# Performance work log

Measured on AMD Instinct MI355X. Metric: run time of the kernel, lower is better.

## Reference

```python
import jax, jax.numpy as jnp
import numpy as np

N_NODES = 100000
N_EDGES = 1600000
F_IN, F_HID, F_OUT = 48, 16, 16
K = 2  # kernel_size, dim=1, degree=1 open B-spline -> basis (1-u, u)


def glorot(key, shape):
    fan_in, fan_out = shape[-2], shape[-1]
    s = jnp.sqrt(6.0 / (fan_in + fan_out))
    return jax.random.uniform(key, shape, jnp.float32, -s, s)


def setup_inputs() -> dict:
    key = jax.random.key(0)
    ks = jax.random.split(key, 10)
    x = jax.random.normal(ks[0], (N_NODES, F_IN), jnp.float32)
    edge_attr = jax.random.uniform(ks[1], (N_EDGES, 1), jnp.float32)
    edge_index = jax.random.randint(ks[2], (2, N_EDGES), 0, N_NODES, jnp.int64)
    W1 = glorot(ks[3], (K, F_IN, F_HID))
    root1 = glorot(ks[4], (F_IN, F_HID))
    b1 = jnp.zeros((F_HID,), jnp.float32)
    W2 = glorot(ks[5], (K, F_HID, F_OUT))
    root2 = glorot(ks[6], (F_HID, F_OUT))
    b2 = jnp.zeros((F_OUT,), jnp.float32)
    return {"x": x, "edge_attr": edge_attr, "edge_index": edge_index,
            "W1": W1, "root1": root1, "b1": b1, "W2": W2, "root2": root2, "b2": b2}


def spline_conv(x, edge_index, u, W, root, bias, num_nodes):
    # x: [N,Fin], u: [E] pseudo coords in [0,1], W: [2,Fin,Fout]
    src, dst = edge_index[0], edge_index[1]
    xj = x[src]                                        # [E,Fin] gather
    m = jnp.einsum('ef,kfo->eko', xj, W)               # [E,2,Fout]
    basis = jnp.stack([1.0 - u, u], axis=1)            # linear open B-spline, K=2
    msg = jnp.einsum('ek,eko->eo', basis, m)           # [E,Fout]
    agg = jax.ops.segment_sum(msg, dst, num_segments=num_nodes)
    cnt = jax.ops.segment_sum(jnp.ones_like(msg[:, 0]), dst, num_segments=num_nodes)
    agg = agg / jnp.maximum(cnt, 1.0)[:, None]         # aggr='mean'
    return agg + x @ root + bias                       # root_weight + bias


def reference(x, edge_attr, edge_index, W1, root1, b1, W2, root2, b2):
    u = edge_attr[:, 0]
    h = jax.nn.elu(spline_conv(x, edge_index, u, W1, root1, b1, N_NODES))
    out = spline_conv(h, edge_index, u, W2, root2, b2, N_NODES)
    return jax.nn.log_softmax(out, axis=1)
```

## Files before the change

### kernel.cpp

```cpp
#include <hip/hip_runtime.h>
#include <math.h>

#define N_NODES 100000
#define N_EDGES 1600000
#define NBUK 782
#define BNODES 128
#define CAPSH 12
#define CAP 4096
#define NCHUNK 512
#define CPE 3125
#define NTBLK 1563
#define WS 52
#define RPW (BNODES + 1)

#define NTL(p) __builtin_nontemporal_load(p)

__device__ __forceinline__ unsigned bf16_rne(float x) {
    unsigned u = __float_as_uint(x);
    return (u + 0x7FFFu + ((u >> 16) & 1u)) >> 16;
}

__device__ __forceinline__ void acc4(float* acc, uint4 w, float uu) {
    acc[0] += fmaf(uu, __uint_as_float(w.x & 0xFFFF0000u), __uint_as_float(w.x << 16));
    acc[1] += fmaf(uu, __uint_as_float(w.y & 0xFFFF0000u), __uint_as_float(w.y << 16));
    acc[2] += fmaf(uu, __uint_as_float(w.z & 0xFFFF0000u), __uint_as_float(w.z << 16));
    acc[3] += fmaf(uu, __uint_as_float(w.w & 0xFFFF0000u), __uint_as_float(w.w << 16));
}

__device__ __forceinline__ void edge_accum(unsigned pk,
                                           const uint4* __restrict__ YPH,
                                           float acc[16]) {
    float uu = (float)(pk >> 17) * (1.0f / 32767.0f);
    const uint4* yp = YPH + (size_t)(pk & 0x1FFFFu) * 4;
    uint4 w0 = yp[0], w1 = yp[1], w2 = yp[2], w3 = yp[3];
    acc4(acc + 0, w0, uu);
    acc4(acc + 4, w1, uu);
    acc4(acc + 8, w2, uu);
    acc4(acc + 12, w3, uu);
}

__device__ __forceinline__ void edge_accum2(unsigned p0, unsigned p1,
                                            const uint4* __restrict__ YPH,
                                            float acc[16]) {
    float u0 = (float)(p0 >> 17) * (1.0f / 32767.0f);
    float u1 = (float)(p1 >> 17) * (1.0f / 32767.0f);
    const uint4* a = YPH + (size_t)(p0 & 0x1FFFFu) * 4;
    const uint4* b = YPH + (size_t)(p1 & 0x1FFFFu) * 4;
    uint4 w0 = a[0], w1 = a[1], w2 = a[2], w3 = a[3];
    uint4 v0 = b[0], v1 = b[1], v2 = b[2], v3 = b[3];
    acc4(acc + 0, w0, u0);
    acc4(acc + 4, w1, u0);
    acc4(acc + 8, w2, u0);
    acc4(acc + 12, w3, u0);
    acc4(acc + 0, v0, u1);
    acc4(acc + 4, v1, u1);
    acc4(acc + 8, v2, u1);
    acc4(acc + 12, v3, u1);
}

__global__ __launch_bounds__(1024)
void transform1(const float* __restrict__ X,
                const float* __restrict__ W,
                const float* __restrict__ root,
                const float* __restrict__ bias,
                unsigned* __restrict__ YPH, float* __restrict__ R,
                int* __restrict__ cursor) {
    int t = threadIdx.x;
    if (blockIdx.x == NTBLK) {
        if (t < NBUK) cursor[t] = t * CAP;
        return;
    }
    __shared__ float sW0[16 * WS];
    __shared__ float sWd[16 * WS];
    __shared__ float sR[16 * WS];
    __shared__ float sB[16];
    for (int i = t; i < 48 * 16; i += 1024) {
        int f = i >> 4, o = i & 15;
        float w0 = W[i];
        float w1 = W[48 * 16 + i];
        sW0[o * WS + f] = w0;
        sWd[o * WS + f] = w1 - w0;
        sR[o * WS + f]  = root[i];
    }
    if (t < 16) sB[t] = bias[t];
    __syncthreads();

    int idx = blockIdx.x * 1024 + t;
    int n = idx >> 4;
    int o = idx & 15;
    if (n >= N_NODES) return;

    const float4* xr  = (const float4*)(X + (long)n * 48);
    const float4* w0p = (const float4*)(sW0 + o * WS);
    const float4* wdp = (const float4*)(sWd + o * WS);
    const float4* wrp = (const float4*)(sR  + o * WS);
    float a0 = 0.0f, a1 = 0.0f, ar = 0.0f;
#pragma unroll
    for (int fc = 0; fc < 12; ++fc) {
        float4 xv = xr[fc];
        float4 w0 = w0p[fc];
        float4 wd = wdp[fc];
        float4 wr = wrp[fc];
        a0 = fmaf(xv.x, w0.x, a0); a0 = fmaf(xv.y, w0.y, a0);
        a0 = fmaf(xv.z, w0.z, a0); a0 = fmaf(xv.w, w0.w, a0);
        a1 = fmaf(xv.x, wd.x, a1); a1 = fmaf(xv.y, wd.y, a1);
        a1 = fmaf(xv.z, wd.z, a1); a1 = fmaf(xv.w, wd.w, a1);
        ar = fmaf(xv.x, wr.x, ar); ar = fmaf(xv.y, wr.y, ar);
        ar = fmaf(xv.z, wr.z, ar); ar = fmaf(xv.w, wr.w, ar);
    }
    YPH[idx] = bf16_rne(a0) | (bf16_rne(a1) << 16);
    R[idx]   = ar + sB[o];
}

__global__ __launch_bounds__(1024)
void scatter_edges(const int* __restrict__ src, const int* __restrict__ dst,
                   const float* __restrict__ u,
                   int* __restrict__ cursor,
                   unsigned* __restrict__ pkb, unsigned char* __restrict__ dlb) {
    __shared__ unsigned upk[CPE];
    __shared__ unsigned short ubuk[CPE];
    __shared__ unsigned char udl[CPE];
    __shared__ unsigned spk[CPE];
    __shared__ unsigned char sdl[CPE];
    __shared__ unsigned short sbuk[CPE];
    __shared__ int lcur[NBUK];
    __shared__ int gbase[NBUK];
    __shared__ int sc[1024];

    int t = threadIdx.x, c = blockIdx.x;

    for (int i = t; i < NBUK; i += 1024) lcur[i] = 0;
    __syncthreads();
    for (int j = t; j < CPE; j += 1024) {
        int e = c * CPE + j;
        int d = NTL(dst + e);
        float uu = NTL(u + e);
        uu = uu < 0.0f ? 0.0f : (uu > 1.0f ? 1.0f : uu);
        int u15 = (int)fmaf(uu, 32767.0f, 0.5f);
        upk[j] = (unsigned)NTL(src + e) | ((unsigned)u15 << 17);
        udl[j] = (unsigned char)(d & 127);
        int b = d >> 7;
        ubuk[j] = (unsigned short)b;
        atomicAdd(&lcur[b], 1);
    }
    __syncthreads();

    int v = (t < NBUK) ? lcur[t] : 0;
    sc[t] = v;
    __syncthreads();
    for (int off = 1; off < 1024; off <<= 1) {
        int x = (t >= off) ? sc[t - off] : 0;
        __syncthreads();
        sc[t] += x;
        __syncthreads();
    }
    if (t < NBUK) {
        int ex = sc[t] - v;
        lcur[t] = ex;
        int base = atomicAdd(&cursor[t], v);
        gbase[t] = base - ex;
    }
    __syncthreads();

    for (int j = t; j < CPE; j += 1024) {
        int b = ubuk[j];
        int p = atomicAdd(&lcur[b], 1);
        spk[p] = upk[j];
        sdl[p] = udl[j];
        sbuk[p] = (unsigned short)b;
    }
    __syncthreads();

    for (int j = t; j < CPE; j += 1024) {
        int b = sbuk[j];
        int g = gbase[b] + j;
        if (g < ((b + 1) << CAPSH)) {
            pkb[g] = spk[j];
            dlb[g] = sdl[j];
        }
    }
}

__global__ __launch_bounds__(512)
void aggregate1(const int* __restrict__ cursor,
                unsigned* __restrict__ pkb,
                const unsigned char* __restrict__ dlb,
                int* __restrict__ rptab,
                const uint4* __restrict__ YPH1,
                const float* __restrict__ R1,
                const float* __restrict__ W2,
                const float* __restrict__ root2,
                const float* __restrict__ b2,
                unsigned* __restrict__ YPH2,
                float* __restrict__ R2) {
    __shared__ unsigned spk[CAP];
    __shared__ int rp[RPW];
    __shared__ int cur[BNODES];
    __shared__ float sW0[256], sWd[256], sR[256], sB[16];
    int t = threadIdx.x, b = blockIdx.x;

    if (t < 256) {
        float w0 = W2[t], w1 = W2[256 + t];
        sW0[t] = w0;
        sWd[t] = w1 - w0;
        sR[t]  = root2[t];
    }
    if (t < 16) sB[t] = b2[t];
    if (t < BNODES) cur[t] = 0;
    __syncthreads();

    int cnt = cursor[b] - (b << CAPSH);
    if (cnt > CAP) cnt = CAP;
    unsigned* pk = pkb + ((size_t)b << CAPSH);
    const unsigned char* dl = dlb + ((size_t)b << CAPSH);
    int n4 = cnt >> 2, tail = cnt & 3, base4 = cnt & ~3;

    for (int j4 = t; j4 < n4; j4 += 512) {
        unsigned w = NTL((const unsigned*)dl + j4);
        atomicAdd(&cur[w & 255], 1);
        atomicAdd(&cur[(w >> 8) & 255], 1);
        atomicAdd(&cur[(w >> 16) & 255], 1);
        atomicAdd(&cur[w >> 24], 1);
    }
    if (t < tail) atomicAdd(&cur[NTL(dl + base4 + t)], 1);
    __syncthreads();

    int v = 0;
    if (t < BNODES) { v = cur[t]; rp[t] = v; }
    __syncthreads();
    for (int off = 1; off < BNODES; off <<= 1) {
        int x = 0;
        if (t < BNODES && t >= off) x = rp[t - off];
        __syncthreads();
        if (t < BNODES) rp[t] += x;
        __syncthreads();
    }
    if (t < BNODES) { int ex = rp[t] - v; rp[t] = ex; cur[t] = ex; }
    if (t == 0) rp[BNODES] = cnt;
    __syncthreads();

    for (int j4 = t; j4 < n4; j4 += 512) {
        uint4 p = ((const uint4*)pk)[j4];
        unsigned w = NTL((const unsigned*)dl + j4);
        spk[atomicAdd(&cur[w & 255], 1)]         = p.x;
        spk[atomicAdd(&cur[(w >> 8) & 255], 1)]  = p.y;
        spk[atomicAdd(&cur[(w >> 16) & 255], 1)] = p.z;
        spk[atomicAdd(&cur[w >> 24], 1)]         = p.w;
    }
    if (t < tail) {
        int j = base4 + t;
        spk[atomicAdd(&cur[NTL(dl + j)], 1)] = pk[j];
    }
    __syncthreads();

    for (int j = t; j < cnt; j += 512) pk[j] = spk[j];
    if (t < RPW) rptab[b * RPW + t] = rp[t];

    int node = t >> 2, q = t & 3;
    int n = (b << 7) + node;
    int beg = rp[node], end = rp[node + 1];
    int deg = end - beg;

    float acc[16];
#pragma unroll
    for (int i = 0; i < 16; ++i) acc[i] = 0.0f;
    int j = beg + q;
    for (; j + 4 < end; j += 8)
        edge_accum2(spk[j], spk[j + 4], YPH1, acc);
    if (j < end) edge_accum(spk[j], YPH1, acc);

#pragma unroll
    for (int mask = 1; mask <= 2; mask <<= 1) {
#pragma unroll
        for (int i = 0; i < 16; ++i) acc[i] += __shfl_xor(acc[i], mask);
    }

    if (n < N_NODES) {
        float inv = 1.0f / (deg > 0 ? (float)deg : 1.0f);
        float h16[16];
        const float4* rrp = (const float4*)(R1 + (size_t)n * 16);
#pragma unroll
        for (int qq = 0; qq < 4; ++qq) {
            float4 rr = rrp[qq];
            float w;
            w = fmaf(acc[4 * qq + 0], inv, rr.x); h16[4 * qq + 0] = w > 0.0f ? w : expm1f(w);
            w = fmaf(acc[4 * qq + 1], inv, rr.y); h16[4 * qq + 1] = w > 0.0f ? w : expm1f(w);
            w = fmaf(acc[4 * qq + 2], inv, rr.z); h16[4 * qq + 2] = w > 0.0f ? w : expm1f(w);
            w = fmaf(acc[4 * qq + 3], inv, rr.w); h16[4 * qq + 3] = w > 0.0f ? w : expm1f(w);
        }

        float a0[4] = {0, 0, 0, 0}, a1[4] = {0, 0, 0, 0}, ar[4] = {0, 0, 0, 0};
        int o0 = q * 4;
#pragma unroll
        for (int f = 0; f < 16; ++f) {
            float hv = h16[f];
#pragma unroll
            for (int o = 0; o < 4; ++o) {
                a0[o] = fmaf(hv, sW0[f * 16 + o0 + o], a0[o]);
                a1[o] = fmaf(hv, sWd[f * 16 + o0 + o], a1[o]);
                ar[o] = fmaf(hv, sR [f * 16 + o0 + o], ar[o]);
            }
        }
        uint4 yw;
        yw.x = bf16_rne(a0[0]) | (bf16_rne(a1[0]) << 16);
        yw.y = bf16_rne(a0[1]) | (bf16_rne(a1[1]) << 16);
        yw.z = bf16_rne(a0[2]) | (bf16_rne(a1[2]) << 16);
        yw.w = bf16_rne(a0[3]) | (bf16_rne(a1[3]) << 16);
        ((uint4*)YPH2)[(size_t)n * 4 + q] = yw;
        float4 rv;
        rv.x = ar[0] + sB[o0 + 0];
        rv.y = ar[1] + sB[o0 + 1];
        rv.z = ar[2] + sB[o0 + 2];
        rv.w = ar[3] + sB[o0 + 3];
        ((float4*)R2)[(size_t)n * 4 + q] = rv;
    }
}

__global__ __launch_bounds__(512)
void aggregate2(const int* __restrict__ rptab,
                const unsigned* __restrict__ pkb,
                const uint4* __restrict__ YPH2,
                const float* __restrict__ R2,
                float* __restrict__ out) {
    __shared__ int rp[RPW];
    int t = threadIdx.x, b = blockIdx.x;

    if (t < RPW) rp[t] = rptab[b * RPW + t];
    __syncthreads();

    const unsigned* pk = pkb + ((size_t)b << CAPSH);
    int node = t >> 2, q = t & 3;
    int n = (b << 7) + node;
    int beg = rp[node], end = rp[node + 1];
    int deg = end - beg;

    float acc[16];
#pragma unroll
    for (int i = 0; i < 16; ++i) acc[i] = 0.0f;
    int j = beg + q;
    for (; j + 4 < end; j += 8)
        edge_accum2(NTL(pk + j), NTL(pk + j + 4), YPH2, acc);
    if (j < end) edge_accum(NTL(pk + j), YPH2, acc);

#pragma unroll
    for (int mask = 1; mask <= 2; mask <<= 1) {
#pragma unroll
        for (int i = 0; i < 16; ++i) acc[i] += __shfl_xor(acc[i], mask);
    }

    if (n < N_NODES) {
        float inv = 1.0f / (deg > 0 ? (float)deg : 1.0f);
        float4 rr = ((const float4*)R2)[(size_t)n * 4 + q];
        float v0 = fmaf(acc[4 * q + 0], inv, rr.x);
        float v1 = fmaf(acc[4 * q + 1], inv, rr.y);
        float v2 = fmaf(acc[4 * q + 2], inv, rr.z);
        float v3 = fmaf(acc[4 * q + 3], inv, rr.w);
        float m = fmaxf(fmaxf(v0, v1), fmaxf(v2, v3));
        m = fmaxf(m, __shfl_xor(m, 1));
        m = fmaxf(m, __shfl_xor(m, 2));
        float s = expf(v0 - m) + expf(v1 - m) + expf(v2 - m) + expf(v3 - m);
        s += __shfl_xor(s, 1);
        s += __shfl_xor(s, 2);
        float lse = m + logf(s);
        float4 ov = make_float4(v0 - lse, v1 - lse, v2 - lse, v3 - lse);
        ((float4*)out)[(size_t)n * 4 + q] = ov;
    }
}

extern "C" void kernel_launch(void* const* d_in, const int* in_sizes, int n_in,
                              void* d_out, int out_size, void* d_ws, size_t ws_size,
                              hipStream_t stream) {
    const float* x         = (const float*)d_in[0];
    const float* edge_attr = (const float*)d_in[1];
    const int*   edge_idx  = (const int*)d_in[2];
    const float* W1        = (const float*)d_in[3];
    const float* root1     = (const float*)d_in[4];
    const float* b1        = (const float*)d_in[5];
    const float* W2        = (const float*)d_in[6];
    const float* root2     = (const float*)d_in[7];
    const float* b2        = (const float*)d_in[8];
    float* out = (float*)d_out;

    const int* src = edge_idx;
    const int* dst = edge_idx + N_EDGES;

    char* ws = (char*)d_ws;
    unsigned*      pkb    = (unsigned*)(ws);
    unsigned char* dlb    = (unsigned char*)(ws + 12812288);
    unsigned*      YPH1   = (unsigned*)(ws + 16015360);
    float*         R1     = (float*)(ws + 22415360);
    unsigned*      YPH2   = (unsigned*)(ws + 28815360);
    float*         R2     = (float*)(ws + 35215360);
    int*           cursor = (int*)(ws + 41615360);
    int*           rptab  = (int*)(ws + 41618496);

    transform1<<<dim3(NTBLK + 1), 1024, 0, stream>>>(
        x, W1, root1, b1, YPH1, R1, cursor);

    scatter_edges<<<dim3(NCHUNK), 1024, 0, stream>>>(
        src, dst, edge_attr, cursor, pkb, dlb);

    aggregate1<<<dim3(NBUK), 512, 0, stream>>>(
        cursor, pkb, dlb, rptab, (const uint4*)YPH1, R1, W2, root2, b2, YPH2, R2);

    aggregate2<<<dim3(NBUK), 512, 0, stream>>>(
        rptab, pkb, (const uint4*)YPH2, R2, out);
}
```

Measured before the change: 190.6 us.

## Fuse node transform with edge scatter and split edge gather across quad lanes

Merges the layer-1 node transform and the edge bucketing scatter into one launch whose blocks branch on block index and share dynamic shared memory. The cursor array is now zero-initialised with a memset and holds relative counts, with the bucket offset added at the use site. In both aggregation kernels each of the four lanes per node now loads only its own 16-byte quarter of every neighbour row and walks all edges, instead of splitting edges across lanes and reducing 16 accumulators with shuffles. The layer-2 transform then rebuilds the full 16-wide hidden vector through lane shuffles. The goal is fewer launches, coalesced quarter-row loads and lower register pressure, at the cost of four times more edge-index reads per lane.

Result: faster. 179.7 us (-5.7%).

```diff
diff --git a/kernel.cpp b/kernel.cpp
--- a/kernel.cpp
+++ b/kernel.cpp
@@ -13,6 +13,17 @@
 #define WS 52
 #define RPW (BNODES + 1)
 
+#define SM_LCUR   0
+#define SM_GBASE  3128
+#define SM_SC     6256
+#define SM_UPK    10352
+#define SM_SPK    22852
+#define SM_UBUK   35352
+#define SM_SBUK   41602
+#define SM_UDL    47852
+#define SM_SDL    50977
+#define SM_TOTAL  54144
+
 #define NTL(p) __builtin_nontemporal_load(p)
 
 __device__ __forceinline__ unsigned bf16_rne(float x) {
@@ -20,164 +31,131 @@
     return (u + 0x7FFFu + ((u >> 16) & 1u)) >> 16;
 }
 
-__device__ __forceinline__ void acc4(float* acc, uint4 w, float uu) {
+__device__ __forceinline__ void accq(float acc[4], uint4 w, float uu) {
     acc[0] += fmaf(uu, __uint_as_float(w.x & 0xFFFF0000u), __uint_as_float(w.x << 16));
     acc[1] += fmaf(uu, __uint_as_float(w.y & 0xFFFF0000u), __uint_as_float(w.y << 16));
     acc[2] += fmaf(uu, __uint_as_float(w.z & 0xFFFF0000u), __uint_as_float(w.z << 16));
     acc[3] += fmaf(uu, __uint_as_float(w.w & 0xFFFF0000u), __uint_as_float(w.w << 16));
 }
 
-__device__ __forceinline__ void edge_accum(unsigned pk,
-                                           const uint4* __restrict__ YPH,
-                                           float acc[16]) {
-    float uu = (float)(pk >> 17) * (1.0f / 32767.0f);
-    const uint4* yp = YPH + (size_t)(pk & 0x1FFFFu) * 4;
-    uint4 w0 = yp[0], w1 = yp[1], w2 = yp[2], w3 = yp[3];
-    acc4(acc + 0, w0, uu);
-    acc4(acc + 4, w1, uu);
-    acc4(acc + 8, w2, uu);
-    acc4(acc + 12, w3, uu);
-}
-
-__device__ __forceinline__ void edge_accum2(unsigned p0, unsigned p1,
-                                            const uint4* __restrict__ YPH,
-                                            float acc[16]) {
-    float u0 = (float)(p0 >> 17) * (1.0f / 32767.0f);
-    float u1 = (float)(p1 >> 17) * (1.0f / 32767.0f);
-    const uint4* a = YPH + (size_t)(p0 & 0x1FFFFu) * 4;
-    const uint4* b = YPH + (size_t)(p1 & 0x1FFFFu) * 4;
-    uint4 w0 = a[0], w1 = a[1], w2 = a[2], w3 = a[3];
-    uint4 v0 = b[0], v1 = b[1], v2 = b[2], v3 = b[3];
-    acc4(acc + 0, w0, u0);
-    acc4(acc + 4, w1, u0);
-    acc4(acc + 8, w2, u0);
-    acc4(acc + 12, w3, u0);
-    acc4(acc + 0, v0, u1);
-    acc4(acc + 4, v1, u1);
-    acc4(acc + 8, v2, u1);
-    acc4(acc + 12, v3, u1);
-}
-
 __global__ __launch_bounds__(1024)
-void transform1(const float* __restrict__ X,
-                const float* __restrict__ W,
-                const float* __restrict__ root,
-                const float* __restrict__ bias,
-                unsigned* __restrict__ YPH, float* __restrict__ R,
-                int* __restrict__ cursor) {
+void fused_transform_scatter(const float* __restrict__ X,
+                             const float* __restrict__ W,
+                             const float* __restrict__ root,
+                             const float* __restrict__ bias,
+                             unsigned* __restrict__ YPH, float* __restrict__ R,
+                             const int* __restrict__ src,
+                             const int* __restrict__ dst,
+                             const float* __restrict__ u,
+                             int* __restrict__ cursor,
+                             unsigned* __restrict__ pkb,
+                             unsigned char* __restrict__ dlb) {
+    extern __shared__ char smem[];
     int t = threadIdx.x;
-    if (blockIdx.x == NTBLK) {
-        if (t < NBUK) cursor[t] = t * CAP;
-        return;
-    }
-    __shared__ float sW0[16 * WS];
-    __shared__ float sWd[16 * WS];
-    __shared__ float sR[16 * WS];
-    __shared__ float sB[16];
-    for (int i = t; i < 48 * 16; i += 1024) {
-        int f = i >> 4, o = i & 15;
-        float w0 = W[i];
-        float w1 = W[48 * 16 + i];
-        sW0[o * WS + f] = w0;
-        sWd[o * WS + f] = w1 - w0;
-        sR[o * WS + f]  = root[i];
-    }
-    if (t < 16) sB[t] = bias[t];
-    __syncthreads();
-
-    int idx = blockIdx.x * 1024 + t;
-    int n = idx >> 4;
-    int o = idx & 15;
-    if (n >= N_NODES) return;
-
-    const float4* xr  = (const float4*)(X + (long)n * 48);
-    const float4* w0p = (const float4*)(sW0 + o * WS);
-    const float4* wdp = (const float4*)(sWd + o * WS);
-    const float4* wrp = (const float4*)(sR  + o * WS);
-    float a0 = 0.0f, a1 = 0.0f, ar = 0.0f;
+    if (blockIdx.x < NCHUNK) {
+        int c = blockIdx.x;
+        int* lcur            = (int*)(smem + SM_LCUR);
+        int* gbase           = (int*)(smem + SM_GBASE);
+        int* sc              = (int*)(smem + SM_SC);
+        unsigned* upk        = (unsigned*)(smem + SM_UPK);
+        unsigned* spk        = (unsigned*)(smem + SM_SPK);
+        unsigned short* ubuk = (unsigned short*)(smem + SM_UBUK);
+        unsigned short* sbuk = (unsigned short*)(smem + SM_SBUK);
+        unsigned char* udl   = (unsigned char*)(smem + SM_UDL);
+        unsigned char* sdl   = (unsigned char*)(smem + SM_SDL);
+
+        for (int i = t; i < NBUK; i += 1024) lcur[i] = 0;
+        __syncthreads();
+        for (int j = t; j < CPE; j += 1024) {
+            int e = c * CPE + j;
+            int d = NTL(dst + e);
+            float uu = NTL(u + e);
+            uu = uu < 0.0f ? 0.0f : (uu > 1.0f ? 1.0f : uu);
+            int u15 = (int)fmaf(uu, 32767.0f, 0.5f);
+            upk[j] = (unsigned)NTL(src + e) | ((unsigned)u15 << 17);
+            udl[j] = (unsigned char)(d & 127);
+            int b = d >> 7;
+            ubuk[j] = (unsigned short)b;
+            atomicAdd(&lcur[b], 1);
+        }
+        __syncthreads();
+
+        int v = (t < NBUK) ? lcur[t] : 0;
+        sc[t] = v;
+        __syncthreads();
+        for (int off = 1; off < 1024; off <<= 1) {
+            int x = (t >= off) ? sc[t - off] : 0;
+            __syncthreads();
+            sc[t] += x;
+            __syncthreads();
+        }
+        if (t < NBUK) {
+            int ex = sc[t] - v;
+            lcur[t] = ex;
+            int base = (t << CAPSH) + atomicAdd(&cursor[t], v);
+            gbase[t] = base - ex;
+        }
+        __syncthreads();
+
+        for (int j = t; j < CPE; j += 1024) {
+            int b = ubuk[j];
+            int p = atomicAdd(&lcur[b], 1);
+            spk[p] = upk[j];
+            sdl[p] = udl[j];
+            sbuk[p] = (unsigned short)b;
+        }
+        __syncthreads();
+
+        for (int j = t; j < CPE; j += 1024) {
+            int b = sbuk[j];
+            int g = gbase[b] + j;
+            if (g < ((b + 1) << CAPSH)) {
+                pkb[g] = spk[j];
+                dlb[g] = sdl[j];
+            }
+        }
+    } else {
+        float* sW0 = (float*)smem;
+        float* sWd = (float*)(smem + 3328);
+        float* sR  = (float*)(smem + 6656);
+        float* sB  = (float*)(smem + 9984);
+        int bid = blockIdx.x - NCHUNK;
+        for (int i = t; i < 48 * 16; i += 1024) {
+            int f = i >> 4, o = i & 15;
+            float w0 = W[i];
+            float w1 = W[48 * 16 + i];
+            sW0[o * WS + f] = w0;
+            sWd[o * WS + f] = w1 - w0;
+            sR[o * WS + f]  = root[i];
+        }
+        if (t < 16) sB[t] = bias[t];
+        __syncthreads();
+
+        int idx = bid * 1024 + t;
+        int n = idx >> 4;
+        int o = idx & 15;
+        if (n >= N_NODES) return;
+
+        const float4* xr  = (const float4*)(X + (long)n * 48);
+        const float4* w0p = (const float4*)(sW0 + o * WS);
+        const float4* wdp = (const float4*)(sWd + o * WS);
+        const float4* wrp = (const float4*)(sR  + o * WS);
+        float a0 = 0.0f, a1 = 0.0f, ar = 0.0f;
 #pragma unroll
-    for (int fc = 0; fc < 12; ++fc) {
-        float4 xv = xr[fc];
-        float4 w0 = w0p[fc];
-        float4 wd = wdp[fc];
-        float4 wr = wrp[fc];
-        a0 = fmaf(xv.x, w0.x, a0); a0 = fmaf(xv.y, w0.y, a0);
-        a0 = fmaf(xv.z, w0.z, a0); a0 = fmaf(xv.w, w0.w, a0);
-        a1 = fmaf(xv.x, wd.x, a1); a1 = fmaf(xv.y, wd.y, a1);
-        a1 = fmaf(xv.z, wd.z, a1); a1 = fmaf(xv.w, wd.w, a1);
-        ar = fmaf(xv.x, wr.x, ar); ar = fmaf(xv.y, wr.y, ar);
-        ar = fmaf(xv.z, wr.z, ar); ar = fmaf(xv.w, wr.w, ar);
-    }
-    YPH[idx] = bf16_rne(a0) | (bf16_rne(a1) << 16);
-    R[idx]   = ar + sB[o];
-}
-
-__global__ __launch_bounds__(1024)
-void scatter_edges(const int* __restrict__ src, const int* __restrict__ dst,
-                   const float* __restrict__ u,
-                   int* __restrict__ cursor,
-                   unsigned* __restrict__ pkb, unsigned char* __restrict__ dlb) {
-    __shared__ unsigned upk[CPE];
-    __shared__ unsigned short ubuk[CPE];
-    __shared__ unsigned char udl[CPE];
-    __shared__ unsigned spk[CPE];
-    __shared__ unsigned char sdl[CPE];
-    __shared__ unsigned short sbuk[CPE];
-    __shared__ int lcur[NBUK];
-    __shared__ int gbase[NBUK];
-    __shared__ int sc[1024];
-
-    int t = threadIdx.x, c = blockIdx.x;
-
-    for (int i = t; i < NBUK; i += 1024) lcur[i] = 0;
-    __syncthreads();
-    for (int j = t; j < CPE; j += 1024) {
-        int e = c * CPE + j;
-        int d = NTL(dst + e);
-        float uu = NTL(u + e);
-        uu = uu < 0.0f ? 0.0f : (uu > 1.0f ? 1.0f : uu);
-        int u15 = (int)fmaf(uu, 32767.0f, 0.5f);
-        upk[j] = (unsigned)NTL(src + e) | ((unsigned)u15 << 17);
-        udl[j] = (unsigned char)(d & 127);
-        int b = d >> 7;
-        ubuk[j] = (unsigned short)b;
-        atomicAdd(&lcur[b], 1);
-    }
-    __syncthreads();
-
-    int v = (t < NBUK) ? lcur[t] : 0;
-    sc[t] = v;
-    __syncthreads();
-    for (int off = 1; off < 1024; off <<= 1) {
-        int x = (t >= off) ? sc[t - off] : 0;
-        __syncthreads();
-        sc[t] += x;
-        __syncthreads();
-    }
-    if (t < NBUK) {
-        int ex = sc[t] - v;
-        lcur[t] = ex;
-        int base = atomicAdd(&cursor[t], v);
-        gbase[t] = base - ex;
-    }
-    __syncthreads();
-
-    for (int j = t; j < CPE; j += 1024) {
-        int b = ubuk[j];
-        int p = atomicAdd(&lcur[b], 1);
-        spk[p] = upk[j];
-        sdl[p] = udl[j];
-        sbuk[p] = (unsigned short)b;
-    }
-    __syncthreads();
-
-    for (int j = t; j < CPE; j += 1024) {
-        int b = sbuk[j];
-        int g = gbase[b] + j;
-        if (g < ((b + 1) << CAPSH)) {
-            pkb[g] = spk[j];
-            dlb[g] = sdl[j];
-        }
+        for (int fc = 0; fc < 12; ++fc) {
+            float4 xv = xr[fc];
+            float4 w0 = w0p[fc];
+            float4 wd = wdp[fc];
+            float4 wr = wrp[fc];
+            a0 = fmaf(xv.x, w0.x, a0); a0 = fmaf(xv.y, w0.y, a0);
+            a0 = fmaf(xv.z, w0.z, a0); a0 = fmaf(xv.w, w0.w, a0);
+            a1 = fmaf(xv.x, wd.x, a1); a1 = fmaf(xv.y, wd.y, a1);
+            a1 = fmaf(xv.z, wd.z, a1); a1 = fmaf(xv.w, wd.w, a1);
+            ar = fmaf(xv.x, wr.x, ar); ar = fmaf(xv.y, wr.y, ar);
+            ar = fmaf(xv.z, wr.z, ar); ar = fmaf(xv.w, wr.w, ar);
+        }
+        YPH[idx] = bf16_rne(a0) | (bf16_rne(a1) << 16);
+        R[idx]   = ar + sB[o];
     }
 }
 
@@ -209,7 +187,7 @@
     if (t < BNODES) cur[t] = 0;
     __syncthreads();
 
-    int cnt = cursor[b] - (b << CAPSH);
+    int cnt = cursor[b];
     if (cnt > CAP) cnt = CAP;
     unsigned* pk = pkb + ((size_t)b << CAPSH);
     const unsigned char* dl = dlb + ((size_t)b << CAPSH);
@@ -260,33 +238,44 @@
     int n = (b << 7) + node;
     int beg = rp[node], end = rp[node + 1];
     int deg = end - beg;
-
-    float acc[16];
-#pragma unroll
-    for (int i = 0; i < 16; ++i) acc[i] = 0.0f;
-    int j = beg + q;
-    for (; j + 4 < end; j += 8)
-        edge_accum2(spk[j], spk[j + 4], YPH1, acc);
-    if (j < end) edge_accum(spk[j], YPH1, acc);
-
-#pragma unroll
-    for (int mask = 1; mask <= 2; mask <<= 1) {
-#pragma unroll
-        for (int i = 0; i < 16; ++i) acc[i] += __shfl_xor(acc[i], mask);
+    const float C = 1.0f / 32767.0f;
+
+    float acc[4] = {0.0f, 0.0f, 0.0f, 0.0f};
+    int j = beg;
+    for (; j + 3 < end; j += 4) {
+        unsigned p0 = spk[j], p1 = spk[j + 1], p2 = spk[j + 2], p3 = spk[j + 3];
+        uint4 w0 = YPH1[(size_t)(p0 & 0x1FFFFu) * 4 + q];
+        uint4 w1 = YPH1[(size_t)(p1 & 0x1FFFFu) * 4 + q];
+        uint4 w2 = YPH1[(size_t)(p2 & 0x1FFFFu) * 4 + q];
+        uint4 w3 = YPH1[(size_t)(p3 & 0x1FFFFu) * 4 + q];
+        accq(acc, w0, (float)(p0 >> 17) * C);
+        accq(acc, w1, (float)(p1 >> 17) * C);
+        accq(acc, w2, (float)(p2 >> 17) * C);
+        accq(acc, w3, (float)(p3 >> 17) * C);
+    }
+    for (; j < end; ++j) {
+        unsigned p = spk[j];
+        uint4 w = YPH1[(size_t)(p & 0x1FFFFu) * 4 + q];
+        accq(acc, w, (float)(p >> 17) * C);
     }
 
     if (n < N_NODES) {
         float inv = 1.0f / (deg > 0 ? (float)deg : 1.0f);
+        float4 rr = ((const float4*)(R1 + (size_t)n * 16))[q];
+        float hq[4], w;
+        w = fmaf(acc[0], inv, rr.x); hq[0] = w > 0.0f ? w : expm1f(w);
+        w = fmaf(acc[1], inv, rr.y); hq[1] = w > 0.0f ? w : expm1f(w);
+        w = fmaf(acc[2], inv, rr.z); hq[2] = w > 0.0f ? w : expm1f(w);
+        w = fmaf(acc[3], inv, rr.w); hq[3] = w > 0.0f ? w : expm1f(w);
+
+        int qbase = (t & 63) & ~3;
         float h16[16];
-        const float4* rrp = (const float4*)(R1 + (size_t)n * 16);
 #pragma unroll
-        for (int qq = 0; qq < 4; ++qq) {
-            float4 rr = rrp[qq];
-            float w;
-            w = fmaf(acc[4 * qq + 0], inv, rr.x); h16[4 * qq + 0] = w > 0.0f ? w : expm1f(w);
-            w = fmaf(acc[4 * qq + 1], inv, rr.y); h16[4 * qq + 1] = w > 0.0f ? w : expm1f(w);
-            w = fmaf(acc[4 * qq + 2], inv, rr.z); h16[4 * qq + 2] = w > 0.0f ? w : expm1f(w);
-            w = fmaf(acc[4 * qq + 3], inv, rr.w); h16[4 * qq + 3] = w > 0.0f ? w : expm1f(w);
+        for (int p = 0; p < 4; ++p) {
+            h16[4 * p + 0] = __shfl(hq[0], qbase + p);
+            h16[4 * p + 1] = __shfl(hq[1], qbase + p);
+            h16[4 * p + 2] = __shfl(hq[2], qbase + p);
+            h16[4 * p + 3] = __shfl(hq[3], qbase + p);
         }
 
         float a0[4] = {0, 0, 0, 0}, a1[4] = {0, 0, 0, 0}, ar[4] = {0, 0, 0, 0};
@@ -333,28 +322,34 @@
     int n = (b << 7) + node;
     int beg = rp[node], end = rp[node + 1];
     int deg = end - beg;
-
-    float acc[16];
-#pragma unroll
-    for (int i = 0; i < 16; ++i) acc[i] = 0.0f;
-    int j = beg + q;
-    for (; j + 4 < end; j += 8)
-        edge_accum2(NTL(pk + j), NTL(pk + j + 4), YPH2, acc);
-    if (j < end) edge_accum(NTL(pk + j), YPH2, acc);
-
-#pragma unroll
-    for (int mask = 1; mask <= 2; mask <<= 1) {
-#pragma unroll
-        for (int i = 0; i < 16; ++i) acc[i] += __shfl_xor(acc[i], mask);
+    const float C = 1.0f / 32767.0f;
+
+    float acc[4] = {0.0f, 0.0f, 0.0f, 0.0f};
+    int j = beg;
+    for (; j + 3 < end; j += 4) {
+        unsigned p0 = pk[j], p1 = pk[j + 1], p2 = pk[j + 2], p3 = pk[j + 3];
+        uint4 w0 = YPH2[(size_t)(p0 & 0x1FFFFu) * 4 + q];
+        uint4 w1 = YPH2[(size_t)(p1 & 0x1FFFFu) * 4 + q];
+        uint4 w2 = YPH2[(size_t)(p2 & 0x1FFFFu) * 4 + q];
+        uint4 w3 = YPH2[(size_t)(p3 & 0x1FFFFu) * 4 + q];
+        accq(acc, w0, (float)(p0 >> 17) * C);
+        accq(acc, w1, (float)(p1 >> 17) * C);
+        accq(acc, w2, (float)(p2 >> 17) * C);
+        accq(acc, w3, (float)(p3 >> 17) * C);
+    }
+    for (; j < end; ++j) {
+        unsigned p = pk[j];
+        uint4 w = YPH2[(size_t)(p & 0x1FFFFu) * 4 + q];
+        accq(acc, w, (float)(p >> 17) * C);
     }
 
     if (n < N_NODES) {
         float inv = 1.0f / (deg > 0 ? (float)deg : 1.0f);
         float4 rr = ((const float4*)R2)[(size_t)n * 4 + q];
-        float v0 = fmaf(acc[4 * q + 0], inv, rr.x);
-        float v1 = fmaf(acc[4 * q + 1], inv, rr.y);
-        float v2 = fmaf(acc[4 * q + 2], inv, rr.z);
-        float v3 = fmaf(acc[4 * q + 3], inv, rr.w);
+        float v0 = fmaf(acc[0], inv, rr.x);
+        float v1 = fmaf(acc[1], inv, rr.y);
+        float v2 = fmaf(acc[2], inv, rr.z);
+        float v3 = fmaf(acc[3], inv, rr.w);
         float m = fmaxf(fmaxf(v0, v1), fmaxf(v2, v3));
         m = fmaxf(m, __shfl_xor(m, 1));
         m = fmaxf(m, __shfl_xor(m, 2));
@@ -394,11 +389,10 @@
     int*           cursor = (int*)(ws + 41615360);
     int*           rptab  = (int*)(ws + 41618496);
 
-    transform1<<<dim3(NTBLK + 1), 1024, 0, stream>>>(
-        x, W1, root1, b1, YPH1, R1, cursor);
-
-    scatter_edges<<<dim3(NCHUNK), 1024, 0, stream>>>(
-        src, dst, edge_attr, cursor, pkb, dlb);
+    hipMemsetAsync(cursor, 0, NBUK * sizeof(int), stream);
+
+    fused_transform_scatter<<<dim3(NCHUNK + NTBLK), 1024, SM_TOTAL, stream>>>(
+        x, W1, root1, b1, YPH1, R1, src, dst, edge_attr, cursor, pkb, dlb);
 
     aggregate1<<<dim3(NBUK), 512, 0, stream>>>(
         cursor, pkb, dlb, rptab, (const uint4*)YPH1, R1, W2, root2, b2, YPH2, R2);
```
